# Kernel optimization log

Hardware: AMD Instinct MI355X
Metric: run time of the kernel (lower is better)

The kernel has to match this reference:

```python
import jax, jax.numpy as jnp
import numpy as np

NUM_GROUPS = 8
MEAN_DEGREE = 32.0
MAX_NUM_ITER = 10
NUM_NODES = 50000
NUM_UND_EDGES = 800000


def setup_inputs() -> dict:
    key = jax.random.key(0)
    k1, k2, k3, k4 = jax.random.split(key, 4)
    src = jax.random.randint(k1, (NUM_UND_EDGES,), 0, NUM_NODES)
    dst = jax.random.randint(k2, (NUM_UND_EDGES,), 0, NUM_NODES)
    # symmetric directed edge list: reverse of directed edge e (< M) is e + M
    edge_index = jnp.stack([jnp.concatenate([src, dst]), jnp.concatenate([dst, src])])  # [2, 2M]
    E = 2 * NUM_UND_EDGES
    edge_attr = jnp.ones((E,), jnp.float32)
    # _init_messages: messages / marginals initialized near uniform 1/q, normalized
    msg = jax.random.uniform(k3, (E, NUM_GROUPS), jnp.float32, 0.5, 1.5)
    message_init = msg / msg.sum(-1, keepdims=True)
    psi = jax.random.uniform(k4, (NUM_NODES, NUM_GROUPS), jnp.float32, 0.5, 1.5)
    psi_init = psi / psi.sum(-1, keepdims=True)
    # beta = log(q / (sqrt(c) - 1) + 1) per __init__
    beta = jnp.float32(np.log(NUM_GROUPS / (np.sqrt(MEAN_DEGREE) - 1.0) + 1.0))
    return {"edge_index": edge_index, "edge_attr": edge_attr,
            "message_init": message_init, "psi_init": psi_init,
            "beta": beta, "num_nodes": NUM_NODES}


def _bp(edge_index, edge_attr, message_init, psi_init, beta, num_nodes):
    E = edge_index.shape[1]
    M = E // 2
    src_n, dst_n = edge_index[0], edge_index[1]
    rev = jnp.concatenate([jnp.arange(M) + M, jnp.arange(M)])  # reverse directed edge
    ones = jnp.ones((E,), message_init.dtype)
    deg = jax.ops.segment_sum(ones, dst_n, num_segments=num_nodes)  # [N]

    def field_of(psi):
        # approximate BP external field h_k = -(beta/N) * sum_i d_i psi_i(k)
        return -(beta / num_nodes) * (deg[:, None] * psi).sum(0)  # [q]

    def step(carry, _):
        msg, psi, h = carry
        # per-edge factor (1 + psi_{k->i}(t) * (e^{beta w} - 1)); log-domain product
        ew = jnp.exp(beta * edge_attr) - 1.0                       # [E]
        log_src = jnp.log1p(msg * ew[:, None])                     # [E, q]
        node_logprod = jax.ops.segment_sum(log_src, dst_n, num_segments=num_nodes)  # [N, q]
        # message i->j: field * prod over incoming k->i except j->i (divide-out reverse edge)
        new_msg = jnp.exp(h[None, :] + node_logprod[src_n] - log_src[rev])
        new_msg = new_msg / new_msg.sum(-1, keepdims=True)
        new_psi = jnp.exp(h[None, :] + node_logprod)
        new_psi = new_psi / new_psi.sum(-1, keepdims=True)
        diff = jnp.max(jnp.abs(new_msg - msg))
        return (new_msg, new_psi, field_of(new_psi)), diff

    h0 = field_of(psi_init)
    (msg, psi, _), diffs = jax.lax.scan(step, (message_init, psi_init, h0), None, length=MAX_NUM_ITER)
    return msg, psi, diffs


def reference(edge_index, edge_attr, message_init, psi_init, beta, num_nodes):
    msg, psi, diffs = _bp(edge_index, edge_attr, message_init, psi_init, beta, num_nodes)
    # module returns (message_map, marginal_psi, csc_map); csc_map is an index cache, omitted
    return (msg, psi)
```

## Files before the change

kernel.cpp:

```cpp
#include <hip/hip_runtime.h>


constexpr int Q = 8;
constexpr int NITER = 10;
constexpr int TB = 256;
constexpr int TBW = 512;
constexpr int WPB = TBW / 64;
constexpr int MAXDEG = 64;
constexpr int NSTRIPE = 64;
constexpr int CSTRIDE = 16;

__global__ void pass1_kernel(const int* __restrict__ dst, int* __restrict__ count,
                             int* __restrict__ p_local, int E) {
    int e = blockIdx.x * TB + threadIdx.x;
    if (e < E) p_local[e] = atomicAdd(&count[(size_t)dst[e] * CSTRIDE], 1);
}

__global__ void scan_kernel(const int* __restrict__ count, int* __restrict__ row_start, int N) {
    __shared__ int sums[1024];
    int tid = threadIdx.x;
    int chunk = (N + 1023) >> 10;
    int lo = min(tid * chunk, N), hi = min(lo + chunk, N);
    int s = 0;
    for (int i = lo; i < hi; ++i) s += count[(size_t)i * CSTRIDE];
    sums[tid] = s;
    __syncthreads();
    for (int off = 1; off < 1024; off <<= 1) {
        int add = (tid >= off) ? sums[tid - off] : 0;
        __syncthreads();
        sums[tid] += add;
        __syncthreads();
    }
    int run = (tid > 0) ? sums[tid - 1] : 0;
    for (int i = lo; i < hi; ++i) { row_start[i] = run; run += count[(size_t)i * CSTRIDE]; }
    if (tid == 1023) row_start[N] = sums[1023];
}

__global__ void aux_kernel(const int* __restrict__ src_row,
                           const int* __restrict__ dst_row,
                           const int* __restrict__ p_local,
                           const int* __restrict__ row_start,
                           const float* __restrict__ edge_attr,
                           const float* __restrict__ beta_p,
                           const float* __restrict__ msg_init,
                           int4* __restrict__ aux4,
                           float* __restrict__ mt0,
                           int M) {
    int e = blockIdx.x * TB + threadIdx.x;
    if (e >= M) return;
    int s0 = src_row[e], d0 = dst_row[e];
    float beta = *beta_p;
    float w  = expf(beta * edge_attr[e])     - 1.0f;
    float wr = expf(beta * edge_attr[e + M]) - 1.0f;
    int p  = row_start[d0] + p_local[e];
    int rp = row_start[s0] + p_local[e + M];
    aux4[p]  = make_int4(rp, __float_as_int(wr), e, 0);
    aux4[rp] = make_int4(p,  __float_as_int(w),  e + M, 0);
    const float4* mp = reinterpret_cast<const float4*>(msg_init + (size_t)e * Q);
    float4 m0 = mp[0], m1 = mp[1];
    float4* op = reinterpret_cast<float4*>(mt0 + (size_t)p * Q);
    op[0] = make_float4(m0.x * w, m0.y * w, m0.z * w, m0.w * w);
    op[1] = make_float4(m1.x * w, m1.y * w, m1.z * w, m1.w * w);
    const float4* mq = reinterpret_cast<const float4*>(msg_init + (size_t)(e + M) * Q);
    float4 r0 = mq[0], r1 = mq[1];
    float4* oq = reinterpret_cast<float4*>(mt0 + (size_t)rp * Q);
    oq[0] = make_float4(r0.x * wr, r0.y * wr, r0.z * wr, r0.w * wr);
    oq[1] = make_float4(r1.x * wr, r1.y * wr, r1.z * wr, r1.w * wr);
}

__global__ void field_kernel(const float* __restrict__ psi,
                             const int* __restrict__ row_start,
                             float* __restrict__ hacc0, int N) {
    int t = blockIdx.x * TB + threadIdx.x;
    int n = t >> 3, k = t & 7;
    float contrib = 0.f;
    if (n < N)
        contrib = (float)(row_start[n + 1] - row_start[n]) * psi[(size_t)n * Q + k];
    contrib += __shfl_xor(contrib, 8);
    contrib += __shfl_xor(contrib, 16);
    contrib += __shfl_xor(contrib, 32);
    if ((threadIdx.x & 63) < Q)
        atomicAdd(&hacc0[(blockIdx.x & (NSTRIPE - 1)) * Q + (threadIdx.x & 7)], contrib);
}

template <bool FINAL>
__global__ __launch_bounds__(TBW) void bp_iter_kernel(
    const float* __restrict__ mt_old,
    const int4*  __restrict__ aux4,
    const int*   __restrict__ row_start,
    const float* __restrict__ beta_p,
    const float* __restrict__ hacc_cur,
    float* __restrict__ hacc_nxt,
    float* __restrict__ hacc_zer,
    float* __restrict__ out,
    float* __restrict__ psi_out,
    int N, int M, float invN) {
    __shared__ float lbuf[WPB][MAXDEG * Q];
    __shared__ int4  auxbuf[WPB][MAXDEG];
    __shared__ float hpart[WPB][Q];
    __shared__ float accQ[Q];
    int tid = threadIdx.x;
    int wave = tid >> 6, lane = tid & 63, es = lane >> 3, k = lane & 7;

    float v = hacc_cur[tid];
    v += __shfl_xor(v, 8);
    v += __shfl_xor(v, 16);
    v += __shfl_xor(v, 32);
    if (lane < Q) hpart[wave][lane] = v;
    if (tid < Q) accQ[tid] = 0.f;
    if (blockIdx.x == 0) hacc_zer[tid] = 0.f;
    __syncthreads();
    float beta = *beta_p;
    float hk = 0.f;
#pragma unroll
    for (int w2 = 0; w2 < WPB; ++w2) hk += hpart[w2][k];
    hk *= -beta * invN;

    int n = blockIdx.x * WPB + wave;
    float contrib = 0.f;
    if (n < N) {
        int lo = row_start[n], hi = row_start[n + 1];
        float acc = 0.f;
        for (int i = lo + es; i < hi; i += 8) {
            int idx = i - lo;
            float mtv = mt_old[(size_t)i * Q + k];
            if (k == 0 && idx < MAXDEG) auxbuf[wave][idx] = aux4[i];
            float l = log1pf(mtv);
            if (idx < MAXDEG) lbuf[wave][idx * Q + k] = l;
            acc += l;
        }
        acc += __shfl_xor(acc, 8);
        acc += __shfl_xor(acc, 16);
        acc += __shfl_xor(acc, 32);
        float nlp = hk + acc;
        float pp = expf(nlp);
        float s = pp;
        s += __shfl_xor(s, 1);
        s += __shfl_xor(s, 2);
        s += __shfl_xor(s, 4);
        pp /= s;
        if (lane < Q) {
            if (FINAL) psi_out[(size_t)n * Q + k] = pp;
            contrib = (float)(hi - lo) * pp;
        }
        for (int i = lo + es; i < hi; i += 8) {
            int idx = i - lo;
            float l = (idx < MAXDEG) ? lbuf[wave][idx * Q + k]
                                     : log1pf(mt_old[(size_t)i * Q + k]);
            float t = expf(nlp - l);
            float ss = t;
            ss += __shfl_xor(ss, 1);
            ss += __shfl_xor(ss, 2);
            ss += __shfl_xor(ss, 4);
            float inv = 1.0f / ss;
            int4 a = (idx < MAXDEG) ? auxbuf[wave][idx] : aux4[i];
            if (FINAL) {
                int oe = (a.z < M) ? (a.z + M) : (a.z - M);
                out[(size_t)oe * Q + k] = t * inv;
            } else {
                out[(size_t)a.x * Q + k] = t * inv * __int_as_float(a.y);
            }
        }
        if (lane < Q) atomicAdd(&accQ[k], contrib);
    }
    __syncthreads();
    if (tid < Q)
        atomicAdd(&hacc_nxt[(blockIdx.x & (NSTRIPE - 1)) * Q + tid], accQ[tid]);
}

extern "C" void kernel_launch(void* const* d_in, const int* in_sizes, int n_in,
                              void* d_out, int out_size, void* d_ws, size_t ws_size,
                              hipStream_t stream) {
    const int*   edge_index = (const int*)d_in[0];
    const float* edge_attr  = (const float*)d_in[1];
    const float* msg_init   = (const float*)d_in[2];
    const float* psi_init   = (const float*)d_in[3];
    const float* beta_p     = (const float*)d_in[4];

    const int E = in_sizes[1];
    const int M = E / 2;
    const int N = in_sizes[3] / Q;

    const int* src = edge_index;
    const int* dst = edge_index + E;

    float* out_msg = (float*)d_out;
    float* out_psi = (float*)d_out + (size_t)E * Q;

    char* ws = (char*)d_ws;
    size_t off = 0;
    auto alloc = [&](size_t bytes) -> void* {
        void* p = (void*)(ws + off);
        off = (off + bytes + 255) & ~(size_t)255;
        return p;
    };
    float* bufA      = (float*)alloc((size_t)E * Q * sizeof(float));
    int4*  aux4      = (int4*)alloc((size_t)E * sizeof(int4));
    int*   p_local   = (int*)alloc((size_t)E * sizeof(int));
    int*   count     = (int*)alloc((size_t)N * CSTRIDE * sizeof(int));
    int*   row_start = (int*)alloc((size_t)(N + 1) * sizeof(int));
    float* hacc3     = (float*)alloc(3 * NSTRIPE * Q * sizeof(float));
    (void)ws_size;

    const int gE   = (E + TB - 1) / TB;
    const int gM   = (M + TB - 1) / TB;
    const int gOct = (N * Q + TB - 1) / TB;
    const int gF   = (N + WPB - 1) / WPB;
    const float invN = 1.0f / (float)N;

    hipMemsetAsync(count, 0, (size_t)N * CSTRIDE * sizeof(int), stream);
    hipMemsetAsync(hacc3, 0, 3 * NSTRIPE * Q * sizeof(float), stream);
    pass1_kernel<<<gE, TB, 0, stream>>>(dst, count, p_local, E);
    scan_kernel<<<1, 1024, 0, stream>>>(count, row_start, N);
    aux_kernel<<<gM, TB, 0, stream>>>(src, dst, p_local, row_start, edge_attr,
                                      beta_p, msg_init, aux4, out_msg, M);
    field_kernel<<<gOct, TB, 0, stream>>>(psi_init, row_start, hacc3, N);

    const float* cur = out_msg;
    float*       alt = bufA;
    for (int t = 0; t < NITER - 1; ++t) {
        bp_iter_kernel<false><<<gF, TBW, 0, stream>>>(
            cur, aux4, row_start, beta_p,
            hacc3 + (size_t)(t % 3) * NSTRIPE * Q,
            hacc3 + (size_t)((t + 1) % 3) * NSTRIPE * Q,
            hacc3 + (size_t)((t + 2) % 3) * NSTRIPE * Q,
            alt, out_psi, N, M, invN);
        float* tmp = (float*)cur; cur = alt; alt = tmp;
    }
    {
        int t = NITER - 1;
        bp_iter_kernel<true><<<gF, TBW, 0, stream>>>(
            cur, aux4, row_start, beta_p,
            hacc3 + (size_t)(t % 3) * NSTRIPE * Q,
            hacc3 + (size_t)((t + 1) % 3) * NSTRIPE * Q,
            hacc3 + (size_t)((t + 2) % 3) * NSTRIPE * Q,
            out_msg, out_psi, N, M, invN);
    }
}
```

Baseline: 951.8 us.

## Replace single-block prefix scan with three-phase multi-block scan

The single-block scan over node degree counts is replaced by a block-local scan across many blocks, a one-wavefront scan of the block sums, and a pass that adds the offsets back. Before, one block of 1024 threads walked serial chunks of about 49 strided counts each. That serial walk ran twice and left the rest of the GPU idle. The change adds two kernel launches and assumes at most 64 blocks, which holds for N=50000 but not for much larger N.

Measured after the change: 848.3 us. 1.12x faster.

```diff
diff --git a/kernel.cpp b/kernel.cpp
--- a/kernel.cpp
+++ b/kernel.cpp
@@ -9,6 +9,7 @@
 constexpr int MAXDEG = 64;
 constexpr int NSTRIPE = 64;
 constexpr int CSTRIDE = 16;
+constexpr int SCB = 1024;
 
 __global__ void pass1_kernel(const int* __restrict__ dst, int* __restrict__ count,
                              int* __restrict__ p_local, int E) {
@@ -16,24 +17,41 @@
     if (e < E) p_local[e] = atomicAdd(&count[(size_t)dst[e] * CSTRIDE], 1);
 }
 
-__global__ void scan_kernel(const int* __restrict__ count, int* __restrict__ row_start, int N) {
-    __shared__ int sums[1024];
+__global__ void scanA_kernel(const int* __restrict__ count, int* __restrict__ row_start,
+                             int* __restrict__ blocksum, int N) {
+    __shared__ int buf[SCB];
     int tid = threadIdx.x;
-    int chunk = (N + 1023) >> 10;
-    int lo = min(tid * chunk, N), hi = min(lo + chunk, N);
-    int s = 0;
-    for (int i = lo; i < hi; ++i) s += count[(size_t)i * CSTRIDE];
-    sums[tid] = s;
+    int gi = blockIdx.x * SCB + tid;
+    int v = (gi < N) ? count[(size_t)gi * CSTRIDE] : 0;
+    buf[tid] = v;
     __syncthreads();
-    for (int off = 1; off < 1024; off <<= 1) {
-        int add = (tid >= off) ? sums[tid - off] : 0;
+    for (int off = 1; off < SCB; off <<= 1) {
+        int add = (tid >= off) ? buf[tid - off] : 0;
         __syncthreads();
-        sums[tid] += add;
+        buf[tid] += add;
         __syncthreads();
     }
-    int run = (tid > 0) ? sums[tid - 1] : 0;
-    for (int i = lo; i < hi; ++i) { row_start[i] = run; run += count[(size_t)i * CSTRIDE]; }
-    if (tid == 1023) row_start[N] = sums[1023];
+    if (gi < N) row_start[gi] = buf[tid] - v;
+    if (tid == SCB - 1) blocksum[blockIdx.x] = buf[tid];
+}
+
+__global__ void scanB_kernel(int* __restrict__ blocksum, int* __restrict__ row_start,
+                             int nblk, int N) {
+    int tid = threadIdx.x;
+    int orig = (tid < nblk) ? blocksum[tid] : 0;
+    int v = orig;
+    for (int off = 1; off < 64; off <<= 1) {
+        int u = __shfl_up(v, off);
+        if (tid >= off) v += u;
+    }
+    if (tid < nblk) blocksum[tid] = v - orig;
+    if (tid == nblk - 1) row_start[N] = v;
+}
+
+__global__ void scanC_kernel(int* __restrict__ row_start, const int* __restrict__ blocksum,
+                             int N) {
+    int gi = blockIdx.x * SCB + threadIdx.x;
+    if (gi < N) row_start[gi] += blocksum[blockIdx.x];
 }
 
 __global__ void aux_kernel(const int* __restrict__ src_row,
@@ -199,6 +217,7 @@
     int*   p_local   = (int*)alloc((size_t)E * sizeof(int));
     int*   count     = (int*)alloc((size_t)N * CSTRIDE * sizeof(int));
     int*   row_start = (int*)alloc((size_t)(N + 1) * sizeof(int));
+    int*   blocksum  = (int*)alloc(64 * sizeof(int));
     float* hacc3     = (float*)alloc(3 * NSTRIPE * Q * sizeof(float));
     (void)ws_size;
 
@@ -206,12 +225,15 @@
     const int gM   = (M + TB - 1) / TB;
     const int gOct = (N * Q + TB - 1) / TB;
     const int gF   = (N + WPB - 1) / WPB;
+    const int nblk = (N + SCB - 1) / SCB;
     const float invN = 1.0f / (float)N;
 
     hipMemsetAsync(count, 0, (size_t)N * CSTRIDE * sizeof(int), stream);
     hipMemsetAsync(hacc3, 0, 3 * NSTRIPE * Q * sizeof(float), stream);
     pass1_kernel<<<gE, TB, 0, stream>>>(dst, count, p_local, E);
-    scan_kernel<<<1, 1024, 0, stream>>>(count, row_start, N);
+    scanA_kernel<<<nblk, SCB, 0, stream>>>(count, row_start, blocksum, N);
+    scanB_kernel<<<1, 64, 0, stream>>>(blocksum, row_start, nblk, N);
+    scanC_kernel<<<nblk, SCB, 0, stream>>>(row_start, blocksum, N);
     aux_kernel<<<gM, TB, 0, stream>>>(src, dst, p_local, row_start, edge_attr,
                                       beta_p, msg_init, aux4, out_msg, M);
     field_kernel<<<gOct, TB, 0, stream>>>(psi_init, row_start, hacc3, N);
```
